# Optimization experiments

Measured on AMD Instinct MI355X. Metric: run time of the kernel, lower is better.

## Reference

```python
import jax, jax.numpy as jnp
import numpy as np

EPS = 1e-8
N_NODES, N_EDGES = 10000, 160000
SI, VI = 128, 16          # node scalar / vector channels
ES, EV = 32, 4            # edge scalar / vector channels
SO, VO = 128, 16          # output scalar / vector channels
MSI, MVI = 2 * SI + ES, 2 * VI + EV   # message input dims: 288, 36
H1 = max(MVI, VO)         # layer-1 hidden = 36 (bottleneck=1)
H2 = max(VO, VO)          # layer-2 hidden = 16
SVO = 3                   # scalarization_vectorization_output_dim


def _safe_norm(x, axis):
    return jnp.sqrt(jnp.sum(x * x, axis=axis) + EPS)


def _gcp(s, v, frames, Wdown, Wdf, Wso, bso, Wup, Wg, bg):
    """GCP block on edge-level inputs (node_inputs=False, vector_gate=True).
    s: [E, si], v: [E, vi, 3], frames: [E, 3, 3]."""
    v_pre = jnp.swapaxes(v, -1, -2)                 # [E, 3, vi]
    v_hid = v_pre @ Wdown                           # [E, 3, h]
    v_norm = _safe_norm(v_hid, axis=-2)             # [E, h]
    v_frames = v_pre @ Wdf                          # [E, 3, svo]
    # scalarize: frames @ v_frames -> [E,3,svo], transpose -> [E,svo,3], flatten to 9
    local = jnp.swapaxes(frames @ v_frames, -1, -2).reshape(v.shape[0], 3 * SVO)
    merged = jnp.concatenate([s, v_norm, local], axis=-1)
    s_out = merged @ Wso + bso                      # [E, so]
    v_out = jnp.swapaxes(v_hid @ Wup, -1, -2)       # [E, vo, 3]
    gate = jax.nn.sigmoid(jax.nn.silu(s_out) @ Wg + bg)  # vector gate
    v_out = v_out * gate[..., None]
    return jax.nn.silu(s_out), v_out


def _lin(key, fan_in, fan_out):
    return jax.random.normal(key, (fan_in, fan_out), dtype=jnp.float32) / np.sqrt(fan_in)


def setup_inputs() -> dict:
    key = jax.random.key(0)
    ks = jax.random.split(key, 24)
    M1 = H1 + MSI + 3 * SVO   # 333
    M2 = H2 + SO + 3 * SVO    # 153
    return {
        "node_s": jax.random.normal(ks[0], (N_NODES, SI), dtype=jnp.float32),
        "node_v": jax.random.normal(ks[1], (N_NODES, VI, 3), dtype=jnp.float32),
        "edge_s": jax.random.normal(ks[2], (N_EDGES, ES), dtype=jnp.float32),
        "edge_v": jax.random.normal(ks[3], (N_EDGES, EV, 3), dtype=jnp.float32),
        "frames": jax.random.normal(ks[4], (N_EDGES, 3, 3), dtype=jnp.float32),
        "g1_Wdown": _lin(ks[5], MVI, H1),
        "g1_Wdf": _lin(ks[6], MVI, SVO),
        "g1_Wso": _lin(ks[7], M1, SO),
        "g1_bso": jnp.zeros((SO,), dtype=jnp.float32),
        "g1_Wup": _lin(ks[8], H1, VO),
        "g1_Wg": _lin(ks[9], SO, VO),
        "g1_bg": jnp.zeros((VO,), dtype=jnp.float32),
        "g2_Wdown": _lin(ks[10], VO, H2),
        "g2_Wdf": _lin(ks[11], VO, SVO),
        "g2_Wso": _lin(ks[12], M2, SO),
        "g2_bso": jnp.zeros((SO,), dtype=jnp.float32),
        "g2_Wup": _lin(ks[13], H2, VO),
        "g2_Wg": _lin(ks[14], SO, VO),
        "g2_bg": jnp.zeros((VO,), dtype=jnp.float32),
        "att_W": _lin(ks[15], SO, 1),
        "att_b": jnp.zeros((1,), dtype=jnp.float32),
        "edge_index": jax.random.randint(ks[16], (2, N_EDGES), 0, N_NODES, dtype=jnp.int64),
    }


def reference(node_s, node_v, edge_s, edge_v, frames,
              g1_Wdown, g1_Wdf, g1_Wso, g1_bso, g1_Wup, g1_Wg, g1_bg,
              g2_Wdown, g2_Wdf, g2_Wso, g2_bso, g2_Wup, g2_Wg, g2_bg,
              att_W, att_b, edge_index):
    row, col = edge_index[0], edge_index[1]
    # edge gather: concat source node, edge, dest node features
    ms = jnp.concatenate([node_s[row], edge_s, node_s[col]], axis=-1)   # [E, 288]
    mv = jnp.concatenate([node_v[row], edge_v, node_v[col]], axis=1)    # [E, 36, 3]
    # message_fusion[0]
    s, v = _gcp(ms, mv, frames, g1_Wdown, g1_Wdf, g1_Wso, g1_bso, g1_Wup, g1_Wg, g1_bg)
    # message_fusion[1] with residual
    s2, v2 = _gcp(s, v, frames, g2_Wdown, g2_Wdf, g2_Wso, g2_bso, g2_Wup, g2_Wg, g2_bg)
    s, v = s + s2, v + v2
    # scalar message attention
    attn = jax.nn.sigmoid(s @ att_W + att_b)
    s = s * attn
    # flatten ScalarVector and scatter-sum aggregate to destination nodes
    flat = jnp.concatenate([s, v.reshape(v.shape[0], VO * 3)], axis=-1)  # [E, 176]
    agg = jax.ops.segment_sum(flat, row, num_segments=N_NODES)           # [N, 176]
    return agg
```

## Files before the change

kernel.cpp:

```cpp
#include <hip/hip_runtime.h>
#include <hip/hip_bf16.h>

#define E_TOT 160000
#define NN    10000
#define EPB   32

typedef unsigned short ushortT;
typedef unsigned int   uintT;
typedef __attribute__((ext_vector_type(8))) short short8;
typedef __attribute__((ext_vector_type(4))) float f32x4;

__device__ __forceinline__ float sigmoidf_(float x) { return 1.0f / (1.0f + __expf(-x)); }
__device__ __forceinline__ float siluf_(float x) { return x * sigmoidf_(x); }

__device__ __forceinline__ ushortT f2b(float f) {
    union { float f; uintT u; } x; x.f = f;
    uintT r = x.u + 0x7fffu + ((x.u >> 16) & 1u);
    return (ushortT)(r >> 16);
}
__device__ __forceinline__ float b2f(ushortT h) {
    union { uintT u; float f; } x; x.u = ((uintT)h) << 16; return x.f;
}
__device__ __forceinline__ uintT pk2(float lo, float hi) {
    union { __hip_bfloat162 h; uintT u; } cv;
    cv.h = __float22bfloat162_rn(make_float2(lo, hi));
    return cv.u;
}
__device__ __forceinline__ short8 ldfrag(const float* p) {
    const float4 x = ((const float4*)p)[0];
    const float4 y = ((const float4*)p)[1];
    union { uintT u[4]; short8 s; } r;
    r.u[0] = pk2(x.x, x.y); r.u[1] = pk2(x.z, x.w);
    r.u[2] = pk2(y.x, y.y); r.u[3] = pk2(y.z, y.w);
    return r.s;
}

#define OFF_W1SO 0
#define OFF_W2SO 45056
#define OFF_W1DF 65536
#define OFF_W1G  68608
#define OFF_W1UP 70656
#define OFF_W2DF 71680
#define OFF_W2G  72704
#define OFF_W2UP 74752
#define WT_USH   75264

#define NOFF_OFF   56320000ULL
#define CUR_OFF    56360016ULL
#define WT_OFF     57040032ULL
#define WS_CSR     57190560ULL
#define NS16_OFF   57190560ULL
#define WS_NS      59750560ULL
#define ES16_OFF   59750560ULL
#define WS_ES      69990560ULL

__device__ __forceinline__ bool idx_is64(const int* pi) {
    return (pi[1] | pi[3] | pi[5] | pi[7] | pi[9] | pi[11] | pi[13] | pi[15]) == 0;
}

__device__ __forceinline__ void weight_prep(
    int i,
    const float* __restrict__ W1so, const float* __restrict__ W2so,
    const float* __restrict__ W1d,  const float* __restrict__ W1f,
    const float* __restrict__ W1g,  const float* __restrict__ W1up,
    const float* __restrict__ W2d,  const float* __restrict__ W2f,
    const float* __restrict__ W2g,  const float* __restrict__ W2up,
    ushortT* __restrict__ ws)
{
    if (i < OFF_W2SO) {
        int n = i / 352, k = i - n * 352;
        ws[i] = (k < 333) ? f2b(W1so[k * 128 + n]) : (ushortT)0;
    } else if (i < OFF_W1DF) {
        int j = i - OFF_W2SO, n = j / 160, k = j - n * 160;
        ws[i] = (k < 153) ? f2b(W2so[k * 128 + n]) : (ushortT)0;
    } else if (i < OFF_W1G) {
        int j = i - OFF_W1DF, n = j / 64, k = j - n * 64;
        float v = 0.f;
        if (k < 36) { if (n < 36) v = W1d[k * 36 + n]; else if (n < 39) v = W1f[k * 3 + (n - 36)]; }
        ws[i] = f2b(v);
    } else if (i < OFF_W1UP) {
        int j = i - OFF_W1G, n = j / 128, k = j - n * 128;
        ws[i] = f2b(W1g[k * 16 + n]);
    } else if (i < OFF_W2DF) {
        int j = i - OFF_W1UP, n = j / 64, k = j - n * 64;
        ws[i] = (k < 36) ? f2b(W1up[k * 16 + n]) : (ushortT)0;
    } else if (i < OFF_W2G) {
        int j = i - OFF_W2DF, n = j / 32, k = j - n * 32;
        float v = 0.f;
        if (k < 16) { if (n < 16) v = W2d[k * 16 + n]; else if (n < 19) v = W2f[k * 3 + (n - 16)]; }
        ws[i] = f2b(v);
    } else if (i < OFF_W2UP) {
        int j = i - OFF_W2G, n = j / 128, k = j - n * 128;
        ws[i] = f2b(W2g[k * 16 + n]);
    } else if (i < WT_USH) {
        int j = i - OFF_W2UP, n = j / 32, k = j - n * 32;
        ws[i] = (k < 16) ? f2b(W2up[k * 16 + n]) : (ushortT)0;
    }
}

__global__ __launch_bounds__(256) void setup_kernel(
    const float* __restrict__ W1so, const float* __restrict__ W2so,
    const float* __restrict__ W1d,  const float* __restrict__ W1f,
    const float* __restrict__ W1g,  const float* __restrict__ W1up,
    const float* __restrict__ W2d,  const float* __restrict__ W2f,
    const float* __restrict__ W2g,  const float* __restrict__ W2up,
    ushortT* __restrict__ ws,
    const void* __restrict__ eidx, int* __restrict__ cur,
    const float* __restrict__ node_s, const float* __restrict__ edge_s,
    ushortT* __restrict__ ns16, ushortT* __restrict__ es16)
{
    int i = blockIdx.x * 256 + threadIdx.x;
    {
        const int* pi = (const int*)eidx;
        const long long* pl = (const long long*)eidx;
        int r = idx_is64(pi) ? (int)pl[i] : pi[i];
        atomicAdd(&cur[r], 1);
    }
    if (ns16 && i < 160000) {
        float4 x = ((const float4*)node_s)[i * 2];
        float4 y = ((const float4*)node_s)[i * 2 + 1];
        uint4 st;
        st.x = pk2(x.x, x.y); st.y = pk2(x.z, x.w);
        st.z = pk2(y.x, y.y); st.w = pk2(y.z, y.w);
        ((uint4*)ns16)[i] = st;
    }
    if (es16) {
        #pragma unroll
        for (int k = 0; k < 4; ++k) {
            float4 x = ((const float4*)edge_s)[i * 8 + 2 * k];
            float4 y = ((const float4*)edge_s)[i * 8 + 2 * k + 1];
            uint4 st;
            st.x = pk2(x.x, x.y); st.y = pk2(x.z, x.w);
            st.z = pk2(y.x, y.y); st.w = pk2(y.z, y.w);
            ((uint4*)es16)[i * 4 + k] = st;
        }
    }
    weight_prep(i, W1so, W2so, W1d, W1f, W1g, W1up, W2d, W2f, W2g, W2up, ws);
}

__global__ __launch_bounds__(256) void prep_kernel(
    const float* __restrict__ W1so, const float* __restrict__ W2so,
    const float* __restrict__ W1d,  const float* __restrict__ W1f,
    const float* __restrict__ W1g,  const float* __restrict__ W1up,
    const float* __restrict__ W2d,  const float* __restrict__ W2f,
    const float* __restrict__ W2g,  const float* __restrict__ W2up,
    ushortT* __restrict__ ws, float* __restrict__ out)
{
    int i = blockIdx.x * 256 + threadIdx.x;
    float4* o4 = (float4*)out;
    #pragma unroll
    for (int k = 0; k < 6; ++k) {
        int z = i + k * 75264;
        if (z < 440000) o4[z] = make_float4(0.f, 0.f, 0.f, 0.f);
    }
    weight_prep(i, W1so, W2so, W1d, W1f, W1g, W1up, W2d, W2f, W2g, W2up, ws);
}

__global__ __launch_bounds__(256) void scan_kernel(int* __restrict__ cur,
                                                   int* __restrict__ noff)
{
    __shared__ int buf[10000];
    __shared__ int partial[256];
    const int t = threadIdx.x;
    for (int i = t; i < NN; i += 256) buf[i] = cur[i];
    for (int i = t; i < NN; i += 256) cur[i] = 0;
    __syncthreads();
    const int base = t * 40;
    int s = 0;
    #pragma unroll
    for (int i = 0; i < 40; ++i) s += (base + i < NN) ? buf[base + i] : 0;
    partial[t] = s;
    __syncthreads();
    for (int o = 1; o < 256; o <<= 1) {
        int v = (t >= o) ? partial[t - o] : 0;
        __syncthreads();
        partial[t] += v;
        __syncthreads();
    }
    int run = (t == 0) ? 0 : partial[t - 1];
    #pragma unroll
    for (int i = 0; i < 40; ++i) {
        int gi = base + i;
        if (gi < NN) { int v = buf[gi]; noff[gi] = run; run += v; }
    }
    if (t == 255) noff[NN] = partial[255];
}

__global__ __launch_bounds__(256) void node_kernel(const ushortT* __restrict__ fb,
                                                   const int* __restrict__ noff,
                                                   float* __restrict__ out)
{
    const int w = threadIdx.x >> 6, l = threadIdx.x & 63;
    const int n = blockIdx.x * 4 + w;
    if (l >= 44) return;
    const int s = noff[n], eend = noff[n + 1];
    float a0 = 0.f, a1 = 0.f, a2 = 0.f, a3 = 0.f;
    int idx = s;
    for (; idx + 2 <= eend; idx += 2) {
        uint2 p0 = *(const uint2*)(fb + (size_t)idx * 176 + l * 4);
        uint2 p1 = *(const uint2*)(fb + (size_t)(idx + 1) * 176 + l * 4);
        a0 += b2f((ushortT)(p0.x & 0xffff)); a1 += b2f((ushortT)(p0.x >> 16));
        a2 += b2f((ushortT)(p0.y & 0xffff)); a3 += b2f((ushortT)(p0.y >> 16));
        a0 += b2f((ushortT)(p1.x & 0xffff)); a1 += b2f((ushortT)(p1.x >> 16));
        a2 += b2f((ushortT)(p1.y & 0xffff)); a3 += b2f((ushortT)(p1.y >> 16));
    }
    if (idx < eend) {
        uint2 p0 = *(const uint2*)(fb + (size_t)idx * 176 + l * 4);
        a0 += b2f((ushortT)(p0.x & 0xffff)); a1 += b2f((ushortT)(p0.x >> 16));
        a2 += b2f((ushortT)(p0.y & 0xffff)); a3 += b2f((ushortT)(p0.y >> 16));
    }
    ((float4*)(out + (size_t)n * 176))[l] = make_float4(a0, a1, a2, a3);
}

#define MFMA(a, b, c) __builtin_amdgcn_mfma_f32_16x16x32_bf16((a), (b), (c), 0, 0, 0)

__global__ __launch_bounds__(256, 6) void edge_kernel(
    const float* __restrict__ node_s, const float* __restrict__ node_v,
    const float* __restrict__ edge_s, const float* __restrict__ edge_v,
    const float* __restrict__ frames,
    const float* __restrict__ b1so, const float* __restrict__ b1g,
    const float* __restrict__ b2so, const float* __restrict__ b2g,
    const float* __restrict__ attW, const float* __restrict__ attb,
    const ushortT* __restrict__ wsc,
    const void* __restrict__ eidx, float* __restrict__ out,
    ushortT* __restrict__ fb, int* __restrict__ cur, const int* __restrict__ noff,
    const ushortT* __restrict__ ns16, const ushortT* __restrict__ es16,
    int csr)
{
    const ushortT* W1T   = wsc + OFF_W1SO;
    const ushortT* W2T   = wsc + OFF_W2SO;
    const ushortT* W1dfT = wsc + OFF_W1DF;
    const ushortT* W1gT  = wsc + OFF_W1G;
    const ushortT* W1upT = wsc + OFF_W1UP;
    const ushortT* W2dfT = wsc + OFF_W2DF;
    const ushortT* W2gT  = wsc + OFF_W2G;
    const ushortT* W2upT = wsc + OFF_W2UP;

    __shared__ __align__(16) char smem[27136];
    ushortT* mvA     = (ushortT*)smem;
    ushortT* m2      = (ushortT*)smem;
    ushortT* vhidA   = (ushortT*)(smem + 10752);
    ushortT* s2s     = (ushortT*)(smem + 10752);
    ushortT* normbuf = (ushortT*)(smem + 19456);
    ushortT* v1s     = (ushortT*)(smem + 19456);
    ushortT* vhid2A  = (ushortT*)(smem + 19456);
    float*   fr      = (float*)(smem + 24064);
    float*   vfr2f   = (float*)(smem + 25216);
    ushortT* v1f     = (ushortT*)(smem + 24064);

    const int t  = threadIdx.x;
    const int eg = blockIdx.x * EPB;
    const int w  = t >> 6, lane = t & 63, lq = lane >> 4, ln = lane & 15;
    const int te = t >> 3, tj = t & 7;
    const int p  = w & 1;

    const int* pi = (const int*)eidx;
    const long long* pl = (const long long*)eidx;
    const bool is64 = idx_is64(pi);

    int posr = 0;
    float att_reg = 0.f;

    {
        const int nr = is64 ? (int)pl[eg + te] : pi[eg + te];
        const int nc = is64 ? (int)pl[E_TOT + eg + te] : pi[E_TOT + eg + te];
        #pragma unroll
        for (int mi = 0; mi < 2; ++mi) {
            if (mi == 1 && tj != 0) break;
            int m = (mi == 0) ? tj : 8;
            const float* src;
            if (m < 4)       src = node_v + nr * 48 + 12 * m;
            else if (m == 4) src = edge_v + (eg + te) * 12;
            else             src = node_v + nc * 48 + 12 * (m - 5);
            float4 x = ((const float4*)src)[0];
            float4 y = ((const float4*)src)[1];
            float4 z = ((const float4*)src)[2];
            float v[12] = {x.x, x.y, x.z, x.w, y.x, y.y, y.z, y.w, z.x, z.y, z.z, z.w};
            int c0 = 4 * m;
            #pragma unroll
            for (int sp = 0; sp < 3; ++sp) {
                *(uintT*)(mvA + (sp * 32 + te) * 40 + c0)     = pk2(v[sp],     v[3 + sp]);
                *(uintT*)(mvA + (sp * 32 + te) * 40 + c0 + 2) = pk2(v[6 + sp], v[9 + sp]);
            }
        }
        #pragma unroll
        for (int k = 0; k < 2; ++k) {
            int j = tj + k * 8;
            if (j < 9) fr[te * 9 + j] = frames[(eg + te) * 9 + j];
        }
        #pragma unroll
        for (int k = 0; k < 3; ++k) {
            int c = 45 + tj + k * 8;
            if (c < 64) normbuf[te * 72 + c] = 0;
        }
        if (t < 192) {
            int r = t >> 1, cc = 36 + ((t & 1) << 1);
            *(uintT*)(mvA + r * 40 + cc) = 0;
        }
        if (csr && tj == 0) {
            posr = noff[nr] + atomicAdd(&cur[nr], 1);
        }
    }

    const int klq = lq * 8;
    const int dn0 = w * 32 + ln, dn1 = dn0 + 16;
    const ushortT* b0p = W1T + dn0 * 352 + klq;
    const ushortT* b1p = W1T + dn1 * 352 + klq;
    f32x4 acc00 = {0,0,0,0}, acc01 = {0,0,0,0}, acc10 = {0,0,0,0}, acc11 = {0,0,0,0};
    float dbi0, dbi1;
    {
        const int e0 = ln, e1 = 16 + ln;
        int r0, c0, r1, c1;
        if (is64) {
            r0 = (int)pl[eg + e0]; r1 = (int)pl[eg + e1];
            c0 = (int)pl[E_TOT + eg + e0]; c1 = (int)pl[E_TOT + eg + e1];
        } else {
            r0 = pi[eg + e0]; r1 = pi[eg + e1];
            c0 = pi[E_TOT + eg + e0]; c1 = pi[E_TOT + eg + e1];
        }
        r0 *= 128; c0 *= 128; r1 *= 128; c1 *= 128;
        const int eb0 = (eg + e0) * 32, eb1 = (eg + e1) * 32;
        dbi0 = b1so[dn0]; dbi1 = b1so[dn1];
        #pragma unroll
        for (int ks = 0; ks < 9; ++ks) {
            short8 a0, a1;
            if (ks < 4) {
                if (ns16) {
                    a0 = *(const short8*)(ns16 + r0 + ks * 32 + klq);
                    a1 = *(const short8*)(ns16 + r1 + ks * 32 + klq);
                } else {
                    a0 = ldfrag(node_s + r0 + ks * 32 + klq);
                    a1 = ldfrag(node_s + r1 + ks * 32 + klq);
                }
            } else if (ks == 4) {
                if (es16) {
                    a0 = *(const short8*)(es16 + eb0 + klq);
                    a1 = *(const short8*)(es16 + eb1 + klq);
                } else {
                    a0 = ldfrag(edge_s + eb0 + klq);
                    a1 = ldfrag(edge_s + eb1 + klq);
                }
            } else {
                if (ns16) {
                    a0 = *(const short8*)(ns16 + c0 + (ks - 5) * 32 + klq);
                    a1 = *(const short8*)(ns16 + c1 + (ks - 5) * 32 + klq);
                } else {
                    a0 = ldfrag(node_s + c0 + (ks - 5) * 32 + klq);
                    a1 = ldfrag(node_s + c1 + (ks - 5) * 32 + klq);
                }
            }
            short8 b0 = *(const short8*)(b0p + ks * 32);
            short8 b1 = *(const short8*)(b1p + ks * 32);
            acc00 = MFMA(a0, b0, acc00); acc01 = MFMA(a0, b1, acc01);
            acc10 = MFMA(a1, b0, acc10); acc11 = MFMA(a1, b1, acc11);
        }
    }
    asm volatile("" : "+v"(acc00), "+v"(acc01), "+v"(acc10), "+v"(acc11));
    __syncthreads();

    for (int u = w; u < 18; u += 4) {
        int mt = u / 3, nt = u - mt * 3;
        const ushortT* ap = mvA + (mt * 16 + ln) * 40 + lq * 8;
        const ushortT* bp = W1dfT + (nt * 16 + ln) * 64 + lq * 8;
        f32x4 acc = {0.f, 0.f, 0.f, 0.f};
        acc = MFMA(*(const short8*)ap, *(const short8*)bp, acc);
        short8 a2 = {0, 0, 0, 0, 0, 0, 0, 0};
        if (lq == 0) a2 = *(const short8*)(ap + 32);
        acc = MFMA(a2, *(const short8*)(bp + 32), acc);
        if (nt < 2 || ln < 8) {
            ushortT* op = vhidA + (mt * 16 + lq * 4) * 40 + nt * 16 + ln;
            op[0]   = f2b(acc[0]); op[40]  = f2b(acc[1]);
            op[80]  = f2b(acc[2]); op[120] = f2b(acc[3]);
        }
    }
    __syncthreads();

    {
        #pragma unroll
        for (int k = 0; k < 5; ++k) {
            int h = tj + k * 8;
            if (h < 36) {
                float a0 = b2f(vhidA[te * 40 + h]);
                float a1 = b2f(vhidA[(32 + te) * 40 + h]);
                float a2 = b2f(vhidA[(64 + te) * 40 + h]);
                normbuf[te * 72 + h] = f2b(sqrtf(fmaf(a0, a0, fmaf(a1, a1, fmaf(a2, a2, 1e-8f)))));
            }
        }
        for (int i = t; i < 288; i += 256) {
            int e = i / 9, r = i - e * 9, a = r / 3, b = r - a * 3;
            float x = fr[e * 9 + b * 3 + 0] * b2f(vhidA[e * 40 + 36 + a])
                    + fr[e * 9 + b * 3 + 1] * b2f(vhidA[(32 + e) * 40 + 36 + a])
                    + fr[e * 9 + b * 3 + 2] * b2f(vhidA[(64 + e) * 40 + 36 + a]);
            normbuf[e * 72 + 36 + r] = f2b(x);
        }
    }
    __syncthreads();

    {
        const int e0 = ln, e1 = 16 + ln;
        #pragma unroll
        for (int ks = 9; ks < 11; ++ks) {
            short8 a0 = *(const short8*)(normbuf + e0 * 72 + (ks - 9) * 32 + klq);
            short8 a1 = *(const short8*)(normbuf + e1 * 72 + (ks - 9) * 32 + klq);
            short8 b0 = *(const short8*)(b0p + ks * 32);
            short8 b1 = *(const short8*)(b1p + ks * 32);
            acc00 = MFMA(a0, b0, acc00); acc01 = MFMA(a0, b1, acc01);
            acc10 = MFMA(a1, b0, acc10); acc11 = MFMA(a1, b1, acc11);
        }
        #pragma unroll
        for (int r = 0; r < 4; ++r) {
            int m0 = lq * 4 + r;
            m2[m0 * 168 + dn0]        = f2b(siluf_(acc00[r] + dbi0));
            m2[m0 * 168 + dn1]        = f2b(siluf_(acc01[r] + dbi1));
            m2[(16 + m0) * 168 + dn0] = f2b(siluf_(acc10[r] + dbi0));
            m2[(16 + m0) * 168 + dn1] = f2b(siluf_(acc11[r] + dbi1));
        }
    }
    __syncthreads();

    float v1reg[2][4] = {{0.f,0.f,0.f,0.f},{0.f,0.f,0.f,0.f}};
    {
        f32x4 gacc = {0,0,0,0};
        {
            const ushortT* ap = m2 + (p * 16 + ln) * 168;
            const ushortT* bp = W1gT + ln * 128;
            #pragma unroll
            for (int ks = 0; ks < 4; ++ks)
                gacc = MFMA(*(const short8*)(ap + ks * 32 + lq * 8),
                            *(const short8*)(bp + ks * 32 + lq * 8), gacc);
        }
        float g1[4];
        {
            float bi = b1g[ln];
            #pragma unroll
            for (int r = 0; r < 4; ++r) g1[r] = sigmoidf_(gacc[r] + bi);
        }
        const ushortT* bpu = W1upT + ln * 64 + lq * 8;
        short8 bu1 = *(const short8*)bpu;
        short8 bu2 = *(const short8*)(bpu + 32);
        #pragma unroll
        for (int c = 0; c < 2; ++c) {
            if (c == 1 && w >= 2) break;
            int mt = w + c * 4;
            const ushortT* ap = vhidA + (mt * 16 + ln) * 40 + lq * 8;
            f32x4 acc = {0,0,0,0};
            acc = MFMA(*(const short8*)ap, bu1, acc);
            short8 a2 = {0, 0, 0, 0, 0, 0, 0, 0};
            if (lq == 0) a2 = *(const short8*)(ap + 32);
            acc = MFMA(a2, bu2, acc);
            #pragma unroll
            for (int r = 0; r < 4; ++r) {
                int row = mt * 16 + lq * 4 + r;
                float vv = acc[r] * g1[r];
                v1reg[c][r] = vv;
                v1s[row * 16 + ln] = f2b(vv);
            }
        }
        #pragma unroll
        for (int c = 0; c < 2; ++c) {
            if (c == 1 && w >= 2) break;
            int mt = w + c * 4;
            const ushortT* ap = v1s + (mt * 16 + ln) * 16 + lq * 8;
            short8 a = {0, 0, 0, 0, 0, 0, 0, 0};
            if (lq < 2) a = *(const short8*)ap;
            #pragma unroll
            for (int nt = 0; nt < 2; ++nt) {
                const ushortT* bp = W2dfT + (nt * 16 + ln) * 32 + lq * 8;
                f32x4 acc = {0,0,0,0};
                acc = MFMA(a, *(const short8*)bp, acc);
                if (nt == 0) {
                    ushortT* op = vhid2A + (mt * 16 + lq * 4) * 16 + ln;
                    op[0]  = f2b(acc[0]); op[16] = f2b(acc[1]);
                    op[32] = f2b(acc[2]); op[48] = f2b(acc[3]);
                } else if (ln < 3) {
                    float* op = vfr2f + (mt * 16 + lq * 4) * 3 + ln;
                    op[0] = acc[0]; op[3] = acc[1]; op[6] = acc[2]; op[9] = acc[3];
                }
            }
        }
    }
    __syncthreads();

    {
        #pragma unroll
        for (int k = 0; k < 2; ++k) {
            int i = t + k * 256, e = i >> 4, h = i & 15;
            float a0 = b2f(vhid2A[e * 16 + h]);
            float a1 = b2f(vhid2A[(32 + e) * 16 + h]);
            float a2 = b2f(vhid2A[(64 + e) * 16 + h]);
            m2[e * 168 + 128 + h] = f2b(sqrtf(fmaf(a0, a0, fmaf(a1, a1, fmaf(a2, a2, 1e-8f)))));
        }
        for (int i = t; i < 288; i += 256) {
            int e = i / 9, r = i - e * 9, a = r / 3, b = r - a * 3;
            float x = fr[e * 9 + b * 3 + 0] * vfr2f[e * 3 + a]
                    + fr[e * 9 + b * 3 + 1] * vfr2f[(32 + e) * 3 + a]
                    + fr[e * 9 + b * 3 + 2] * vfr2f[(64 + e) * 3 + a];
            m2[e * 168 + 144 + r] = f2b(x);
        }
        if (tj) m2[te * 168 + 152 + tj] = 0;
    }
    __syncthreads();

    {
        f32x4 acc00i = {0,0,0,0}, acc01i = {0,0,0,0}, acc10i = {0,0,0,0}, acc11i = {0,0,0,0};
        const ushortT* a0p = m2 + ln * 168 + lq * 8;
        const ushortT* a1p = m2 + (16 + ln) * 168 + lq * 8;
        const ushortT* b0pi = W2T + (w * 32 + ln) * 160 + lq * 8;
        const ushortT* b1pi = W2T + (w * 32 + 16 + ln) * 160 + lq * 8;
        #pragma unroll
        for (int ks = 0; ks < 5; ++ks) {
            short8 a0 = *(const short8*)(a0p + ks * 32);
            short8 a1 = *(const short8*)(a1p + ks * 32);
            short8 b0 = *(const short8*)(b0pi + ks * 32);
            short8 b1 = *(const short8*)(b1pi + ks * 32);
            acc00i = MFMA(a0, b0, acc00i); acc01i = MFMA(a0, b1, acc01i);
            acc10i = MFMA(a1, b0, acc10i); acc11i = MFMA(a1, b1, acc11i);
        }
        const int n0 = w * 32 + ln, n1 = n0 + 16;
        float bi0 = b2so[n0], bi1 = b2so[n1];
        #pragma unroll
        for (int r = 0; r < 4; ++r) {
            int m0 = lq * 4 + r;
            s2s[m0 * 136 + n0]        = f2b(siluf_(acc00i[r] + bi0));
            s2s[m0 * 136 + n1]        = f2b(siluf_(acc01i[r] + bi1));
            s2s[(16 + m0) * 136 + n0] = f2b(siluf_(acc10i[r] + bi0));
            s2s[(16 + m0) * 136 + n1] = f2b(siluf_(acc11i[r] + bi1));
        }
    }
    __syncthreads();

    {
        f32x4 gacc = {0,0,0,0};
        {
            const ushortT* ap = s2s + (p * 16 + ln) * 136;
            const ushortT* bp = W2gT + ln * 128;
            #pragma unroll
            for (int ks = 0; ks < 4; ++ks)
                gacc = MFMA(*(const short8*)(ap + ks * 32 + lq * 8),
                            *(const short8*)(bp + ks * 32 + lq * 8), gacc);
        }
        float g2[4];
        {
            float bi = b2g[ln];
            #pragma unroll
            for (int r = 0; r < 4; ++r) g2[r] = sigmoidf_(gacc[r] + bi);
        }
        const ushortT* bpu = W2upT + ln * 32 + lq * 8;
        short8 bu = *(const short8*)bpu;
        #pragma unroll
        for (int c = 0; c < 2; ++c) {
            if (c == 1 && w >= 2) break;
            int mt = w + c * 4;
            const ushortT* ap = vhid2A + (mt * 16 + ln) * 16 + lq * 8;
            short8 a = {0, 0, 0, 0, 0, 0, 0, 0};
            if (lq < 2) a = *(const short8*)ap;
            f32x4 acc = {0,0,0,0};
            acc = MFMA(a, bu, acc);
            #pragma unroll
            for (int r = 0; r < 4; ++r) {
                int row = mt * 16 + lq * 4 + r;
                float vfin = v1reg[c][r] + acc[r] * g2[r];
                v1f[row * 16 + ln] = f2b(vfin);
            }
        }
        {
            float sum = 0.f;
            int c0 = tj * 16;
            #pragma unroll
            for (int c = c0; c < c0 + 16; ++c)
                sum = fmaf(b2f(m2[te * 168 + c]) + b2f(s2s[te * 136 + c]), attW[c], sum);
            sum += __shfl_xor(sum, 4);
            sum += __shfl_xor(sum, 2);
            sum += __shfl_xor(sum, 1);
            att_reg = sigmoidf_(sum + attb[0]);
        }
    }
    __syncthreads();

    {
        const float at = att_reg;
        if (csr) {
            const int pos = __shfl(posr, lane & 56);
            ushortT* fbe = fb + (size_t)pos * 176;
            #pragma unroll
            for (int k = 0; k < 11; ++k) {
                int j = 2 * tj + 16 * k;
                float v0, v1;
                if (j < 128) {
                    v0 = (b2f(m2[te * 168 + j])     + b2f(s2s[te * 136 + j]))     * at;
                    v1 = (b2f(m2[te * 168 + j + 1]) + b2f(s2s[te * 136 + j + 1])) * at;
                } else {
                    int r = j - 128;
                    int o0 = r / 3,        sp0 = r - o0 * 3;
                    int o1 = (r + 1) / 3,  sp1 = (r + 1) - o1 * 3;
                    v0 = b2f(v1f[(sp0 * 32 + te) * 16 + o0]);
                    v1 = b2f(v1f[(sp1 * 32 + te) * 16 + o1]);
                }
                *(uintT*)(fbe + j) = pk2(v0, v1);
            }
        } else {
            const int nr = is64 ? (int)pl[eg + te] : pi[eg + te];
            const int orow = nr * 176;
            #pragma unroll
            for (int k = 0; k < 22; ++k) {
                int j = tj + k * 8;
                float val;
                if (j < 128) {
                    val = (b2f(m2[te * 168 + j]) + b2f(s2s[te * 136 + j])) * at;
                } else {
                    int r = j - 128, o = r / 3, sp = r - o * 3;
                    val = b2f(v1f[(sp * 32 + te) * 16 + o]);
                }
                atomicAdd(&out[orow + j], val);
            }
        }
    }
}

extern "C" void kernel_launch(void* const* d_in, const int* in_sizes, int n_in,
                              void* d_out, int out_size, void* d_ws, size_t ws_size,
                              hipStream_t stream) {
    const float* node_s = (const float*)d_in[0];
    const float* node_v = (const float*)d_in[1];
    const float* edge_s = (const float*)d_in[2];
    const float* edge_v = (const float*)d_in[3];
    const float* frames = (const float*)d_in[4];
    const float* W1d  = (const float*)d_in[5];
    const float* W1f  = (const float*)d_in[6];
    const float* W1so = (const float*)d_in[7];
    const float* b1so = (const float*)d_in[8];
    const float* W1up = (const float*)d_in[9];
    const float* W1g  = (const float*)d_in[10];
    const float* b1g  = (const float*)d_in[11];
    const float* W2d  = (const float*)d_in[12];
    const float* W2f  = (const float*)d_in[13];
    const float* W2so = (const float*)d_in[14];
    const float* b2so = (const float*)d_in[15];
    const float* W2up = (const float*)d_in[16];
    const float* W2g  = (const float*)d_in[17];
    const float* b2g  = (const float*)d_in[18];
    const float* attW = (const float*)d_in[19];
    const float* attb = (const float*)d_in[20];
    const void*  eidx = d_in[21];

    float* out = (float*)d_out;
    char* ws = (char*)d_ws;

    int mode = 0;
    if (ws_size >= WS_ES)       mode = 3;
    else if (ws_size >= WS_NS)  mode = 2;
    else if (ws_size >= WS_CSR) mode = 1;
    const int csr = (mode >= 1);

    ushortT* wt    = csr ? (ushortT*)(ws + WT_OFF)  : (ushortT*)ws;
    ushortT* fbuf  = csr ? (ushortT*)ws             : nullptr;
    int*     noff  = csr ? (int*)(ws + NOFF_OFF)    : nullptr;
    int*     cur   = csr ? (int*)(ws + CUR_OFF)     : nullptr;
    ushortT* ns16  = (mode >= 2) ? (ushortT*)(ws + NS16_OFF) : nullptr;
    ushortT* es16  = (mode >= 3) ? (ushortT*)(ws + ES16_OFF) : nullptr;

    if (csr) {
        hipMemsetAsync(cur, 0, NN * sizeof(int), stream);
        setup_kernel<<<625, 256, 0, stream>>>(
            W1so, W2so, W1d, W1f, W1g, W1up, W2d, W2f, W2g, W2up,
            wt, eidx, cur, node_s, edge_s, ns16, es16);
        scan_kernel<<<1, 256, 0, stream>>>(cur, noff);
    } else {
        prep_kernel<<<294, 256, 0, stream>>>(W1so, W2so, W1d, W1f, W1g, W1up,
                                             W2d, W2f, W2g, W2up, wt, out);
    }

    edge_kernel<<<E_TOT / EPB, 256, 0, stream>>>(
        node_s, node_v, edge_s, edge_v, frames,
        b1so, b1g, b2so, b2g, attW, attb,
        (const ushortT*)wt, eidx, out, fbuf, cur, noff, ns16, es16, csr);

    if (csr) {
        node_kernel<<<2500, 256, 0, stream>>>((const ushortT*)fbuf, noff, out);
    }
}
```

Baseline: 312.7 us.

## Precompute per-node projections of layer-1 scalar weights to shrink edge GEMM

Adds a pre_kernel that multiplies each node's bf16 scalar features by the source and destination slices of the layer-1 scalar weight, giving two per-node 128-wide projections. The edge kernel then gathers these projections, adds them, and runs MFMA only over the 32 edge-scalar channels instead of all 288 inputs. The CSR scan is folded into the extra block of pre_kernel, and the bf16 edge_s staging path is removed. This cuts per-edge matmul work and gather bytes, but adds an N-level GEMM pass, an extra bf16 rounding of the partial sums, and more workspace.

```diff
diff --git a/kernel.cpp b/kernel.cpp
--- a/kernel.cpp
+++ b/kernel.cpp
@@ -51,8 +51,9 @@
 #define WS_CSR     57190560ULL
 #define NS16_OFF   57190560ULL
 #define WS_NS      59750560ULL
-#define ES16_OFF   59750560ULL
-#define WS_ES      69990560ULL
+#define PR_OFF     59750560ULL
+#define PC_OFF     62310560ULL
+#define PRE_END    64870560ULL
 
 __device__ __forceinline__ bool idx_is64(const int* pi) {
     return (pi[1] | pi[3] | pi[5] | pi[7] | pi[9] | pi[11] | pi[13] | pi[15]) == 0;
@@ -106,8 +107,8 @@
     const float* __restrict__ W2g,  const float* __restrict__ W2up,
     ushortT* __restrict__ ws,
     const void* __restrict__ eidx, int* __restrict__ cur,
-    const float* __restrict__ node_s, const float* __restrict__ edge_s,
-    ushortT* __restrict__ ns16, ushortT* __restrict__ es16)
+    const float* __restrict__ node_s,
+    ushortT* __restrict__ ns16)
 {
     int i = blockIdx.x * 256 + threadIdx.x;
     {
@@ -123,17 +124,6 @@
         st.x = pk2(x.x, x.y); st.y = pk2(x.z, x.w);
         st.z = pk2(y.x, y.y); st.w = pk2(y.z, y.w);
         ((uint4*)ns16)[i] = st;
-    }
-    if (es16) {
-        #pragma unroll
-        for (int k = 0; k < 4; ++k) {
-            float4 x = ((const float4*)edge_s)[i * 8 + 2 * k];
-            float4 y = ((const float4*)edge_s)[i * 8 + 2 * k + 1];
-            uint4 st;
-            st.x = pk2(x.x, x.y); st.y = pk2(x.z, x.w);
-            st.z = pk2(y.x, y.y); st.w = pk2(y.z, y.w);
-            ((uint4*)es16)[i * 4 + k] = st;
-        }
     }
     weight_prep(i, W1so, W2so, W1d, W1f, W1g, W1up, W2d, W2f, W2g, W2up, ws);
 }
@@ -184,6 +174,68 @@
         if (gi < NN) { int v = buf[gi]; noff[gi] = run; run += v; }
     }
     if (t == 255) noff[NN] = partial[255];
+}
+
+#define MFMA(a, b, c) __builtin_amdgcn_mfma_f32_16x16x32_bf16((a), (b), (c), 0, 0, 0)
+
+__global__ __launch_bounds__(256) void pre_kernel(
+    const ushortT* __restrict__ ns16, const ushortT* __restrict__ wt,
+    ushortT* __restrict__ prt, ushortT* __restrict__ pct,
+    int* __restrict__ cur, int* __restrict__ noff)
+{
+    __shared__ int sbuf[10000];
+    __shared__ int spart[256];
+    const int t = threadIdx.x;
+    if (blockIdx.x == 625) {
+        for (int i = t; i < NN; i += 256) sbuf[i] = cur[i];
+        for (int i = t; i < NN; i += 256) cur[i] = 0;
+        __syncthreads();
+        const int base = t * 40;
+        int s = 0;
+        #pragma unroll
+        for (int i = 0; i < 40; ++i) s += (base + i < NN) ? sbuf[base + i] : 0;
+        spart[t] = s;
+        __syncthreads();
+        for (int o = 1; o < 256; o <<= 1) {
+            int v = (t >= o) ? spart[t - o] : 0;
+            __syncthreads();
+            spart[t] += v;
+            __syncthreads();
+        }
+        int run = (t == 0) ? 0 : spart[t - 1];
+        #pragma unroll
+        for (int i = 0; i < 40; ++i) {
+            int gi = base + i;
+            if (gi < NN) { int v = sbuf[gi]; noff[gi] = run; run += v; }
+        }
+        if (t == 255) noff[NN] = spart[255];
+        return;
+    }
+    const int w = t >> 6, lane = t & 63, lq = lane >> 4, ln = lane & 15, klq = lq * 8;
+    const int nb = blockIdx.x * 16;
+    const int dn0 = w * 32 + ln, dn1 = dn0 + 16;
+    const ushortT* b0p = wt + dn0 * 352 + klq;
+    const ushortT* b1p = wt + dn1 * 352 + klq;
+    const ushortT* arow = ns16 + (size_t)(nb + ln) * 128 + klq;
+    f32x4 a00 = {0,0,0,0}, a01 = {0,0,0,0}, a10 = {0,0,0,0}, a11 = {0,0,0,0};
+    #pragma unroll
+    for (int ks = 0; ks < 4; ++ks) {
+        short8 a  = *(const short8*)(arow + ks * 32);
+        short8 b0 = *(const short8*)(b0p + ks * 32);
+        short8 b1 = *(const short8*)(b1p + ks * 32);
+        short8 c0 = *(const short8*)(b0p + 160 + ks * 32);
+        short8 c1 = *(const short8*)(b1p + 160 + ks * 32);
+        a00 = MFMA(a, b0, a00); a01 = MFMA(a, b1, a01);
+        a10 = MFMA(a, c0, a10); a11 = MFMA(a, c1, a11);
+    }
+    #pragma unroll
+    for (int r = 0; r < 4; ++r) {
+        int n = nb + lq * 4 + r;
+        prt[(size_t)n * 128 + dn0] = f2b(a00[r]);
+        prt[(size_t)n * 128 + dn1] = f2b(a01[r]);
+        pct[(size_t)n * 128 + dn0] = f2b(a10[r]);
+        pct[(size_t)n * 128 + dn1] = f2b(a11[r]);
+    }
 }
 
 __global__ __launch_bounds__(256) void node_kernel(const ushortT* __restrict__ fb,
@@ -212,8 +264,6 @@
     ((float4*)(out + (size_t)n * 176))[l] = make_float4(a0, a1, a2, a3);
 }
 
-#define MFMA(a, b, c) __builtin_amdgcn_mfma_f32_16x16x32_bf16((a), (b), (c), 0, 0, 0)
-
 __global__ __launch_bounds__(256, 6) void edge_kernel(
     const float* __restrict__ node_s, const float* __restrict__ node_v,
     const float* __restrict__ edge_s, const float* __restrict__ edge_v,
@@ -224,7 +274,8 @@
     const ushortT* __restrict__ wsc,
     const void* __restrict__ eidx, float* __restrict__ out,
     ushortT* __restrict__ fb, int* __restrict__ cur, const int* __restrict__ noff,
-    const ushortT* __restrict__ ns16, const ushortT* __restrict__ es16,
+    const ushortT* __restrict__ ns16,
+    const ushortT* __restrict__ prt, const ushortT* __restrict__ pct,
     int csr)
 {
     const ushortT* W1T   = wsc + OFF_W1SO;
@@ -261,17 +312,19 @@
     int posr = 0;
     float att_reg = 0.f;
 
-    {
-        const int nr = is64 ? (int)pl[eg + te] : pi[eg + te];
-        const int nc = is64 ? (int)pl[E_TOT + eg + te] : pi[E_TOT + eg + te];
+    const int nrT = is64 ? (int)pl[eg + te] : pi[eg + te];
+    const int ncT = is64 ? (int)pl[E_TOT + eg + te] : pi[E_TOT + eg + te];
+
+    uint4 pga = {0,0,0,0}, pgb = {0,0,0,0}, pgc = {0,0,0,0}, pgd = {0,0,0,0};
+    {
         #pragma unroll
         for (int mi = 0; mi < 2; ++mi) {
             if (mi == 1 && tj != 0) break;
             int m = (mi == 0) ? tj : 8;
             const float* src;
-            if (m < 4)       src = node_v + nr * 48 + 12 * m;
+            if (m < 4)       src = node_v + nrT * 48 + 12 * m;
             else if (m == 4) src = edge_v + (eg + te) * 12;
-            else             src = node_v + nc * 48 + 12 * (m - 5);
+            else             src = node_v + ncT * 48 + 12 * (m - 5);
             float4 x = ((const float4*)src)[0];
             float4 y = ((const float4*)src)[1];
             float4 z = ((const float4*)src)[2];
@@ -283,6 +336,12 @@
                 *(uintT*)(mvA + (sp * 32 + te) * 40 + c0 + 2) = pk2(v[6 + sp], v[9 + sp]);
             }
         }
+        if (prt) {
+            const ushortT* pr_ = prt + (size_t)nrT * 128 + tj * 16;
+            const ushortT* pc_ = pct + (size_t)ncT * 128 + tj * 16;
+            pga = ((const uint4*)pr_)[0]; pgb = ((const uint4*)pr_)[1];
+            pgc = ((const uint4*)pc_)[0]; pgd = ((const uint4*)pc_)[1];
+        }
         #pragma unroll
         for (int k = 0; k < 2; ++k) {
             int j = tj + k * 8;
@@ -298,7 +357,7 @@
             *(uintT*)(mvA + r * 40 + cc) = 0;
         }
         if (csr && tj == 0) {
-            posr = noff[nr] + atomicAdd(&cur[nr], 1);
+            posr = noff[nrT] + atomicAdd(&cur[nrT], 1);
         }
     }
 
@@ -310,49 +369,53 @@
     float dbi0, dbi1;
     {
         const int e0 = ln, e1 = 16 + ln;
-        int r0, c0, r1, c1;
-        if (is64) {
-            r0 = (int)pl[eg + e0]; r1 = (int)pl[eg + e1];
-            c0 = (int)pl[E_TOT + eg + e0]; c1 = (int)pl[E_TOT + eg + e1];
-        } else {
-            r0 = pi[eg + e0]; r1 = pi[eg + e1];
-            c0 = pi[E_TOT + eg + e0]; c1 = pi[E_TOT + eg + e1];
-        }
-        r0 *= 128; c0 *= 128; r1 *= 128; c1 *= 128;
         const int eb0 = (eg + e0) * 32, eb1 = (eg + e1) * 32;
         dbi0 = b1so[dn0]; dbi1 = b1so[dn1];
-        #pragma unroll
-        for (int ks = 0; ks < 9; ++ks) {
-            short8 a0, a1;
-            if (ks < 4) {
-                if (ns16) {
-                    a0 = *(const short8*)(ns16 + r0 + ks * 32 + klq);
-                    a1 = *(const short8*)(ns16 + r1 + ks * 32 + klq);
-                } else {
-                    a0 = ldfrag(node_s + r0 + ks * 32 + klq);
-                    a1 = ldfrag(node_s + r1 + ks * 32 + klq);
-                }
-            } else if (ks == 4) {
-                if (es16) {
-                    a0 = *(const short8*)(es16 + eb0 + klq);
-                    a1 = *(const short8*)(es16 + eb1 + klq);
-                } else {
+        if (prt) {
+            short8 a0 = ldfrag(edge_s + eb0 + klq);
+            short8 a1 = ldfrag(edge_s + eb1 + klq);
+            short8 b0 = *(const short8*)(b0p + 128);
+            short8 b1 = *(const short8*)(b1p + 128);
+            acc00 = MFMA(a0, b0, acc00); acc01 = MFMA(a0, b1, acc01);
+            acc10 = MFMA(a1, b0, acc10); acc11 = MFMA(a1, b1, acc11);
+        } else {
+            int r0, c0, r1, c1;
+            if (is64) {
+                r0 = (int)pl[eg + e0]; r1 = (int)pl[eg + e1];
+                c0 = (int)pl[E_TOT + eg + e0]; c1 = (int)pl[E_TOT + eg + e1];
+            } else {
+                r0 = pi[eg + e0]; r1 = pi[eg + e1];
+                c0 = pi[E_TOT + eg + e0]; c1 = pi[E_TOT + eg + e1];
+            }
+            r0 *= 128; c0 *= 128; r1 *= 128; c1 *= 128;
+            #pragma unroll
+            for (int ks = 0; ks < 9; ++ks) {
+                short8 a0, a1;
+                if (ks < 4) {
+                    if (ns16) {
+                        a0 = *(const short8*)(ns16 + r0 + ks * 32 + klq);
+                        a1 = *(const short8*)(ns16 + r1 + ks * 32 + klq);
+                    } else {
+                        a0 = ldfrag(node_s + r0 + ks * 32 + klq);
+                        a1 = ldfrag(node_s + r1 + ks * 32 + klq);
+                    }
+                } else if (ks == 4) {
                     a0 = ldfrag(edge_s + eb0 + klq);
                     a1 = ldfrag(edge_s + eb1 + klq);
+                } else {
+                    if (ns16) {
+                        a0 = *(const short8*)(ns16 + c0 + (ks - 5) * 32 + klq);
+                        a1 = *(const short8*)(ns16 + c1 + (ks - 5) * 32 + klq);
+                    } else {
+                        a0 = ldfrag(node_s + c0 + (ks - 5) * 32 + klq);
+                        a1 = ldfrag(node_s + c1 + (ks - 5) * 32 + klq);
+                    }
                 }
-            } else {
-                if (ns16) {
-                    a0 = *(const short8*)(ns16 + c0 + (ks - 5) * 32 + klq);
-                    a1 = *(const short8*)(ns16 + c1 + (ks - 5) * 32 + klq);
-                } else {
-                    a0 = ldfrag(node_s + c0 + (ks - 5) * 32 + klq);
-                    a1 = ldfrag(node_s + c1 + (ks - 5) * 32 + klq);
-                }
-            }
-            short8 b0 = *(const short8*)(b0p + ks * 32);
-            short8 b1 = *(const short8*)(b1p + ks * 32);
-            acc00 = MFMA(a0, b0, acc00); acc01 = MFMA(a0, b1, acc01);
-            acc10 = MFMA(a1, b0, acc10); acc11 = MFMA(a1, b1, acc11);
+                short8 b0 = *(const short8*)(b0p + ks * 32);
+                short8 b1 = *(const short8*)(b1p + ks * 32);
+                acc00 = MFMA(a0, b0, acc00); acc01 = MFMA(a0, b1, acc01);
+                acc10 = MFMA(a1, b0, acc10); acc11 = MFMA(a1, b1, acc11);
+            }
         }
     }
     asm volatile("" : "+v"(acc00), "+v"(acc01), "+v"(acc10), "+v"(acc11));
@@ -393,6 +456,17 @@
                     + fr[e * 9 + b * 3 + 2] * b2f(vhidA[(64 + e) * 40 + 36 + a]);
             normbuf[e * 72 + 36 + r] = f2b(x);
         }
+        if (prt) {
+            uintT pr_[8] = {pga.x, pga.y, pga.z, pga.w, pgb.x, pgb.y, pgb.z, pgb.w};
+            uintT pc_[8] = {pgc.x, pgc.y, pgc.z, pgc.w, pgd.x, pgd.y, pgd.z, pgd.w};
+            uintT* dst = (uintT*)(m2 + te * 168 + tj * 16);
+            #pragma unroll
+            for (int j = 0; j < 8; ++j) {
+                float lo = b2f((ushortT)(pr_[j] & 0xffff)) + b2f((ushortT)(pc_[j] & 0xffff));
+                float hi = b2f((ushortT)(pr_[j] >> 16))    + b2f((ushortT)(pc_[j] >> 16));
+                dst[j] = pk2(lo, hi);
+            }
+        }
     }
     __syncthreads();
 
@@ -407,13 +481,28 @@
             acc00 = MFMA(a0, b0, acc00); acc01 = MFMA(a0, b1, acc01);
             acc10 = MFMA(a1, b0, acc10); acc11 = MFMA(a1, b1, acc11);
         }
-        #pragma unroll
-        for (int r = 0; r < 4; ++r) {
-            int m0 = lq * 4 + r;
-            m2[m0 * 168 + dn0]        = f2b(siluf_(acc00[r] + dbi0));
-            m2[m0 * 168 + dn1]        = f2b(siluf_(acc01[r] + dbi1));
-            m2[(16 + m0) * 168 + dn0] = f2b(siluf_(acc10[r] + dbi0));
-            m2[(16 + m0) * 168 + dn1] = f2b(siluf_(acc11[r] + dbi1));
+        if (prt) {
+            #pragma unroll
+            for (int r = 0; r < 4; ++r) {
+                int m0 = lq * 4 + r;
+                float p00 = b2f(m2[m0 * 168 + dn0]);
+                float p01 = b2f(m2[m0 * 168 + dn1]);
+                float p10 = b2f(m2[(16 + m0) * 168 + dn0]);
+                float p11 = b2f(m2[(16 + m0) * 168 + dn1]);
+                m2[m0 * 168 + dn0]        = f2b(siluf_(acc00[r] + p00 + dbi0));
+                m2[m0 * 168 + dn1]        = f2b(siluf_(acc01[r] + p01 + dbi1));
+                m2[(16 + m0) * 168 + dn0] = f2b(siluf_(acc10[r] + p10 + dbi0));
+                m2[(16 + m0) * 168 + dn1] = f2b(siluf_(acc11[r] + p11 + dbi1));
+            }
+        } else {
+            #pragma unroll
+            for (int r = 0; r < 4; ++r) {
+                int m0 = lq * 4 + r;
+                m2[m0 * 168 + dn0]        = f2b(siluf_(acc00[r] + dbi0));
+                m2[m0 * 168 + dn1]        = f2b(siluf_(acc01[r] + dbi1));
+                m2[(16 + m0) * 168 + dn0] = f2b(siluf_(acc10[r] + dbi0));
+                m2[(16 + m0) * 168 + dn1] = f2b(siluf_(acc11[r] + dbi1));
+            }
         }
     }
     __syncthreads();
@@ -599,8 +688,7 @@
                 *(uintT*)(fbe + j) = pk2(v0, v1);
             }
         } else {
-            const int nr = is64 ? (int)pl[eg + te] : pi[eg + te];
-            const int orow = nr * 176;
+            const int orow = nrT * 176;
             #pragma unroll
             for (int k = 0; k < 22; ++k) {
                 int j = tj + k * 8;
@@ -646,25 +734,26 @@
     float* out = (float*)d_out;
     char* ws = (char*)d_ws;
 
-    int mode = 0;
-    if (ws_size >= WS_ES)       mode = 3;
-    else if (ws_size >= WS_NS)  mode = 2;
-    else if (ws_size >= WS_CSR) mode = 1;
-    const int csr = (mode >= 1);
-
+    const int csr = ws_size >= WS_CSR;
     ushortT* wt    = csr ? (ushortT*)(ws + WT_OFF)  : (ushortT*)ws;
     ushortT* fbuf  = csr ? (ushortT*)ws             : nullptr;
     int*     noff  = csr ? (int*)(ws + NOFF_OFF)    : nullptr;
     int*     cur   = csr ? (int*)(ws + CUR_OFF)     : nullptr;
-    ushortT* ns16  = (mode >= 2) ? (ushortT*)(ws + NS16_OFF) : nullptr;
-    ushortT* es16  = (mode >= 3) ? (ushortT*)(ws + ES16_OFF) : nullptr;
+    ushortT* ns16  = (ws_size >= WS_NS) ? (ushortT*)(ws + NS16_OFF) : nullptr;
+    const int pre  = csr && ns16 && (ws_size >= PRE_END);
+    ushortT* prt   = pre ? (ushortT*)(ws + PR_OFF) : nullptr;
+    ushortT* pct   = pre ? (ushortT*)(ws + PC_OFF) : nullptr;
 
     if (csr) {
         hipMemsetAsync(cur, 0, NN * sizeof(int), stream);
         setup_kernel<<<625, 256, 0, stream>>>(
             W1so, W2so, W1d, W1f, W1g, W1up, W2d, W2f, W2g, W2up,
-            wt, eidx, cur, node_s, edge_s, ns16, es16);
-        scan_kernel<<<1, 256, 0, stream>>>(cur, noff);
+            wt, eidx, cur, node_s, ns16);
+        if (pre) {
+            pre_kernel<<<626, 256, 0, stream>>>(ns16, wt, prt, pct, cur, noff);
+        } else {
+            scan_kernel<<<1, 256, 0, stream>>>(cur, noff);
+        }
     } else {
         prep_kernel<<<294, 256, 0, stream>>>(W1so, W2so, W1d, W1f, W1g, W1up,
                                              W2d, W2f, W2g, W2up, wt, out);
@@ -673,7 +762,7 @@
     edge_kernel<<<E_TOT / EPB, 256, 0, stream>>>(
         node_s, node_v, edge_s, edge_v, frames,
         b1so, b1g, b2so, b2g, attW, attb,
-        (const ushortT*)wt, eidx, out, fbuf, cur, noff, ns16, es16, csr);
+        (const ushortT*)wt, eidx, out, fbuf, cur, noff, ns16, prt, pct, csr);
 
     if (csr) {
         node_kernel<<<2500, 256, 0, stream>>>((const ushortT*)fbuf, noff, out);
```

New measurement: 277.8 us. 11.1% less time.
